# Performance work log

Hardware: AMD Instinct MI355X
Metric: run time of the kernel (lower is better)

Reference implementation:

```python
import jax, jax.numpy as jnp
import numpy as np


def setup_inputs() -> dict:
    key = jax.random.key(0)
    ks = jax.random.split(key, 10)
    B, T, F, C, D, O = 4, 1000, 257, 6, 2048, 2
    # target_doas in DEGREES (module multiplies by pi/180): azi in [0,360), zenith in [0,180)
    tdoa = jax.random.uniform(ks[2], (B, T, 2), dtype=jnp.float32) * jnp.array([360.0, 180.0], jnp.float32)
    # codebook dirs in RADIANS: azi in [0,2pi), zenith in [0,pi)
    dirs = jax.random.uniform(ks[3], (D, 2), dtype=jnp.float32) * jnp.array([2.0 * np.pi, np.pi], jnp.float32)
    return {
        "X_real": jax.random.normal(ks[0], (B, T, F, C), dtype=jnp.float32),
        "X_imag": jax.random.normal(ks[1], (B, T, F, C), dtype=jnp.float32),
        "target_doas": tdoa,
        "dirs": dirs,
        "w_conj_real": jax.random.normal(ks[4], (C, F, D), dtype=jnp.float32),
        "w_conj_imag": jax.random.normal(ks[5], (C, F, D), dtype=jnp.float32),
        "w_conj_ds_real": jax.random.normal(ks[6], (C, F, D), dtype=jnp.float32),
        "w_conj_ds_imag": jax.random.normal(ks[7], (C, F, D), dtype=jnp.float32),
        "w_binaural_real": jax.random.normal(ks[8], (O, F, D), dtype=jnp.float32),
        "w_binaural_imag": jax.random.normal(ks[9], (O, F, D), dtype=jnp.float32),
    }


def _as_ri(z):
    # complex -> stacked (real, imag) float array on last axis
    return jnp.stack([jnp.real(z), jnp.imag(z)], axis=-1)


def reference(X_real, X_imag, target_doas, dirs,
              w_conj_real, w_conj_imag,
              w_conj_ds_real, w_conj_ds_imag,
              w_binaural_real, w_binaural_imag):
    # --- angular (haversine) distance to direction codebook ---
    t = (jnp.pi / 180.0) * target_doas            # [B,T,2] radians
    azi_diff = t[..., 0][:, :, None] - dirs[:, 0][None, None, :]      # [B,T,D]
    zen_diff = t[..., 1][:, :, None] - dirs[:, 1][None, None, :]      # [B,T,D]
    a = jnp.sin(zen_diff / 2) ** 2 + \
        jnp.cos(t[..., 1])[:, :, None] * jnp.cos(dirs[:, 1])[None, None, :] * jnp.sin(azi_diff / 2) ** 2
    angle_diff = 2.0 * jnp.arcsin(jnp.sqrt(jnp.clip(a, 0.0, 1.0)))
    ind = jnp.argmin(angle_diff, axis=-1)          # [B,T] nearest-codebook index

    # --- gather complex beamformer weights by index: [C,F,D] -> [B,T,F,C] ---
    def gather(w):
        return jnp.transpose(w[:, :, ind], (2, 3, 1, 0))

    X = jax.lax.complex(X_real, X_imag)                                 # [B,T,F,C]
    w_conj = jax.lax.complex(gather(w_conj_real), gather(w_conj_imag))  # [B,T,F,C]
    w_ds = jax.lax.complex(gather(w_conj_ds_real), gather(w_conj_ds_imag))
    w_bin = jax.lax.complex(gather(w_binaural_real), gather(w_binaural_imag))  # [B,T,F,O]

    ds_multichannel_out = w_ds * X                 # [B,T,F,C]
    bf_out = jnp.sum(w_conj * X, axis=-1)          # [B,T,F]
    return (_as_ri(ds_multichannel_out), _as_ri(bf_out), _as_ri(w_bin))
```

## Files before the change

kernel.cpp:

```cpp
#include <hip/hip_runtime.h>
#include <math.h>

typedef float f4v __attribute__((ext_vector_type(4)));
typedef float f2v __attribute__((ext_vector_type(2)));

constexpr int Bn = 4, Tn = 1000, Fn = 257, Cn = 6, Dn = 2048, On = 2;
constexpr int BTn = Bn * Tn;
constexpr double DEG2RAD = 0.017453292519943295;

constexpr size_t OUT0_F = (size_t)BTn * Fn * Cn * 2;
constexpr size_t OUT1_F = (size_t)BTn * Fn * 2;

constexpr int DCH = 32;
constexpr int NCH = Dn / DCH;
constexpr int FCH = 8;
constexpr int RWS = FCH * Cn;
constexpr int FCB = 24;
constexpr int RWB = FCB * On;
constexpr int YCD = (Fn + FCH - 1) / FCH;
constexpr int YB  = (Fn + FCB - 1) / FCB;
constexpr int DPAD = 34;
constexpr int NT = 512;

constexpr size_t TAB_BYTES  = (size_t)4 * Dn * sizeof(double);
constexpr size_t BTT_PAD    = 131072;
constexpr size_t IND_BYTES  = 16384;
constexpr size_t BOFF_BYTES = 4096;
constexpr size_t BENT_BYTES = 16384;
constexpr size_t WS_NEEDED  = TAB_BYTES + BTT_PAD + IND_BYTES + BOFF_BYTES + BENT_BYTES;

__global__ __launch_bounds__(256) void build_tables(const float2* __restrict__ dirs,
                                                    const float* __restrict__ tdoa,
                                                    double* __restrict__ tab,
                                                    double* __restrict__ bttab) {
    int id = blockIdx.x * 256 + threadIdx.x;
    if (id < Dn) {
        float2 dr = dirs[id];
        double d0 = (double)dr.x, d1 = (double)dr.y;
        tab[0 * Dn + id] = cos(d0);
        tab[1 * Dn + id] = sin(d0);
        tab[2 * Dn + id] = cos(d1);
        tab[3 * Dn + id] = sin(d1);
    } else if (id < Dn + BTn) {
        int bt = id - Dn;
        double t0 = DEG2RAD * (double)tdoa[bt * 2 + 0];
        double t1 = DEG2RAD * (double)tdoa[bt * 2 + 1];
        bttab[bt * 4 + 0] = cos(t0);
        bttab[bt * 4 + 1] = sin(t0);
        bttab[bt * 4 + 2] = cos(t1);
        bttab[bt * 4 + 3] = sin(t1);
    }
}

__global__ __launch_bounds__(256) void argmin_lds(const double* __restrict__ bttab,
                                                  const double* __restrict__ tab,
                                                  int* __restrict__ ind) {
    __shared__ double s_cd0[Dn];
    __shared__ double s_sd0[Dn];
    __shared__ double s_cd1[Dn];
    __shared__ double s_sd1[Dn];
    const int t = threadIdx.x;
    #pragma unroll
    for (int k = 0; k < Dn / 256; ++k) {
        int d = t + 256 * k;
        s_cd0[d] = tab[0 * Dn + d];
        s_sd0[d] = tab[1 * Dn + d];
        s_cd1[d] = tab[2 * Dn + d];
        s_sd1[d] = tab[3 * Dn + d];
    }
    __syncthreads();
    const int w = t >> 6, lane = t & 63;
    #pragma unroll
    for (int s = 0; s < 4; ++s) {
        const int bt = blockIdx.x * 16 + w * 4 + s;
        double ct0 = bttab[bt * 4 + 0], st0 = bttab[bt * 4 + 1];
        double ct1 = bttab[bt * 4 + 2], st1 = bttab[bt * 4 + 3];
        double best = 1e300;
        int bidx = 0;
        for (int i = 0; i < Dn / 256; ++i) {
            const int d0 = lane + 256 * i;
            double a[4];
            #pragma unroll
            for (int k = 0; k < 4; ++k) {
                int d = d0 + 64 * k;
                double u  = ct1 * s_cd1[d];
                double m1 = 1.0 - (u + st1 * s_sd1[d]);
                double m0 = 1.0 - (ct0 * s_cd0[d] + st0 * s_sd0[d]);
                a[k] = m1 + u * m0;
            }
            #pragma unroll
            for (int k = 0; k < 4; ++k) {
                int d = d0 + 64 * k;
                if (a[k] < best) { best = a[k]; bidx = d; }
            }
        }
        #pragma unroll
        for (int off = 32; off > 0; off >>= 1) {
            double ov = __shfl_down(best, off);
            int oi = __shfl_down(bidx, off);
            if (ov < best || (ov == best && oi < bidx)) { best = ov; bidx = oi; }
        }
        if (lane == 0) ind[bt] = bidx;
    }
}

__global__ __launch_bounds__(256) void bucket_bts(const int* __restrict__ ind,
                                                  int* __restrict__ boff,
                                                  int* __restrict__ bent) {
    __shared__ int cnts[NCH];
    __shared__ int curs[NCH];
    const int t = threadIdx.x;
    if (t < NCH) cnts[t] = 0;
    __syncthreads();
    #pragma unroll
    for (int k = 0; k < (BTn + 255) / 256; ++k) {
        int bt = k * 256 + t;
        if (bt < BTn) atomicAdd(&cnts[ind[bt] >> 5], 1);
    }
    __syncthreads();
    if (t == 0) {
        int acc = 0;
        for (int i = 0; i < NCH; ++i) { curs[i] = acc; boff[i] = acc; acc += cnts[i]; }
        boff[NCH] = acc;
    }
    __syncthreads();
    #pragma unroll
    for (int k = 0; k < (BTn + 255) / 256; ++k) {
        int bt = k * 256 + t;
        if (bt < BTn) {
            int d = ind[bt];
            int p = atomicAdd(&curs[d >> 5], 1);
            bent[p] = (bt << 5) | (d & 31);
        }
    }
}

__global__ __launch_bounds__(NT) void fuse_all(
    const float* __restrict__ Xr, const float* __restrict__ Xi,
    const int* __restrict__ boff, const int* __restrict__ bent,
    const float* __restrict__ wcr, const float* __restrict__ wci,
    const float* __restrict__ wdr, const float* __restrict__ wdi,
    const float* __restrict__ wbr, const float* __restrict__ wbi,
    float* __restrict__ out0, float* __restrict__ out1, float* __restrict__ out2) {
    __shared__ __align__(16) char smem[2 * RWS * DPAD * sizeof(f2v)];
    const int bx = blockIdx.x;
    const int d0 = bx * DCH;
    const int t = threadIdx.x;
    const int off = boff[bx];
    const int cnt = boff[bx + 1] - off;

    if (blockIdx.y < YCD) {
        f2v (*tc)[DPAD] = (f2v(*)[DPAD])smem;
        f2v (*td)[DPAD] = (f2v(*)[DPAD])(smem + sizeof(f2v) * RWS * DPAD);
        const int f0 = blockIdx.y * FCH;
        const int items = cnt * FCH;

        bool vA = false; int btA = 0, fA = 0, dlA = 0, rbA = 0;
        f2v xrA0 = {0,0}, xrA1 = {0,0}, xrA2 = {0,0};
        f2v xiA0 = {0,0}, xiA1 = {0,0}, xiA2 = {0,0};
        if (t < items) {
            int e = bent[off + (t >> 3)];
            int fi = t & 7, f = f0 + fi;
            if (f < Fn) {
                vA = true; btA = e >> 5; fA = f; dlA = e & 31; rbA = fi * Cn;
                size_t xb = ((size_t)btA * Fn + f) * Cn;
                const f2v* xr2 = (const f2v*)(Xr + xb);
                const f2v* xi2 = (const f2v*)(Xi + xb);
                xrA0 = xr2[0]; xrA1 = xr2[1]; xrA2 = xr2[2];
                xiA0 = xi2[0]; xiA1 = xi2[1]; xiA2 = xi2[2];
            }
        }
        #pragma unroll
        for (int j = 0; j < 2; ++j) {
            int idx = j * NT + t;
            if (idx < 768) {
                const int pair = (idx >= 384) ? 1 : 0;
                int k = idx - pair * 384;
                int r = k >> 3, q4 = k & 7;
                int fi = r / Cn, c = r - fi * Cn;
                int f = f0 + fi;
                if (f < Fn) {
                    size_t s = (size_t)(c * Fn + f) * Dn + d0 + 4 * q4;
                    f4v vr = *(const f4v*)((pair ? wdr : wcr) + s);
                    f4v vi = *(const f4v*)((pair ? wdi : wci) + s);
                    f4v* trow = (f4v*)&(pair ? td : tc)[r][0];
                    f4v lo = {vr[0], vi[0], vr[1], vi[1]};
                    f4v hi = {vr[2], vi[2], vr[3], vi[3]};
                    trow[2 * q4]     = lo;
                    trow[2 * q4 + 1] = hi;
                }
            }
        }
        __syncthreads();

        for (int base = 0; base < items; base += NT) {
            bool vB = false; int btB = 0, fB = 0, dlB = 0, rbB = 0;
            f2v xrB0 = {0,0}, xrB1 = {0,0}, xrB2 = {0,0};
            f2v xiB0 = {0,0}, xiB1 = {0,0}, xiB2 = {0,0};
            int itn = base + NT + t;
            if (itn < items) {
                int e = bent[off + (itn >> 3)];
                int fi = itn & 7, f = f0 + fi;
                if (f < Fn) {
                    vB = true; btB = e >> 5; fB = f; dlB = e & 31; rbB = fi * Cn;
                    size_t xb = ((size_t)btB * Fn + f) * Cn;
                    const f2v* xr2 = (const f2v*)(Xr + xb);
                    const f2v* xi2 = (const f2v*)(Xi + xb);
                    xrB0 = xr2[0]; xrB1 = xr2[1]; xrB2 = xr2[2];
                    xiB0 = xi2[0]; xiB1 = xi2[1]; xiB2 = xi2[2];
                }
            }
            if (vA) {
                float xr[Cn] = {xrA0[0], xrA0[1], xrA1[0], xrA1[1], xrA2[0], xrA2[1]};
                float xi[Cn] = {xiA0[0], xiA0[1], xiA1[0], xiA1[1], xiA2[0], xiA2[1]};
                float o0[Cn * 2];
                float accr = 0.f, acci = 0.f;
                #pragma unroll
                for (int c = 0; c < Cn; ++c) {
                    f2v wcv = tc[rbA + c][dlA];
                    f2v wdv = td[rbA + c][dlA];
                    o0[2 * c]     = wdv[0] * xr[c] - wdv[1] * xi[c];
                    o0[2 * c + 1] = wdv[0] * xi[c] + wdv[1] * xr[c];
                    accr += wcv[0] * xr[c] - wcv[1] * xi[c];
                    acci += wcv[0] * xi[c] + wcv[1] * xr[c];
                }
                size_t xb = ((size_t)btA * Fn + fA) * Cn;
                f4v* ob = (f4v*)(out0 + xb * 2);
                f4v p0 = {o0[0], o0[1], o0[2], o0[3]};
                f4v p1 = {o0[4], o0[5], o0[6], o0[7]};
                f4v p2 = {o0[8], o0[9], o0[10], o0[11]};
                ob[0] = p0; ob[1] = p1; ob[2] = p2;
                f2v o1 = {accr, acci};
                ((f2v*)out1)[(size_t)btA * Fn + fA] = o1;
            }
            vA = vB; btA = btB; fA = fB; dlA = dlB; rbA = rbB;
            xrA0 = xrB0; xrA1 = xrB1; xrA2 = xrB2;
            xiA0 = xiB0; xiA1 = xiB1; xiA2 = xiB2;
        }
    } else {
        f2v (*tb)[DPAD] = (f2v(*)[DPAD])smem;
        const int f0 = (blockIdx.y - YCD) * FCB;
        {
            int idx = t;
            if (idx < RWB * 8) {
                int r = idx >> 3, q4 = idx & 7;
                int fi = r >> 1, o = r & 1;
                int f = f0 + fi;
                if (f < Fn) {
                    size_t s = (size_t)(o * Fn + f) * Dn + d0 + 4 * q4;
                    f4v vr = *(const f4v*)(wbr + s);
                    f4v vi = *(const f4v*)(wbi + s);
                    f4v* trow = (f4v*)&tb[r][0];
                    f4v lo = {vr[0], vi[0], vr[1], vi[1]};
                    f4v hi = {vr[2], vi[2], vr[3], vi[3]};
                    trow[2 * q4]     = lo;
                    trow[2 * q4 + 1] = hi;
                }
            }
        }
        __syncthreads();
        const int items = cnt * FCB;
        for (int base = 0; base < items; base += NT) {
            int it = base + t;
            if (it < items) {
                int m = it / FCB, fi = it - m * FCB;
                int e = bent[off + m];
                int bt = e >> 5, dl = e & 31;
                int f = f0 + fi;
                if (f < Fn) {
                    f2v a = tb[fi * 2][dl];
                    f2v b = tb[fi * 2 + 1][dl];
                    f4v o2 = {a[0], a[1], b[0], b[1]};
                    ((f4v*)out2)[(size_t)bt * Fn + f] = o2;
                }
            }
        }
    }
}

__global__ __launch_bounds__(256) void main_direct(
    const float* __restrict__ Xr, const float* __restrict__ Xi,
    const float* __restrict__ tdoa, const float2* __restrict__ dirs,
    const float* __restrict__ wcr, const float* __restrict__ wci,
    const float* __restrict__ wdr, const float* __restrict__ wdi,
    const float* __restrict__ wbr, const float* __restrict__ wbi,
    float2* __restrict__ out0, float2* __restrict__ out1, float2* __restrict__ out2) {
    const int bt = blockIdx.x;
    const int tid = threadIdx.x;
    __shared__ double sv[256];
    __shared__ int si[256];

    double t0 = DEG2RAD * (double)tdoa[bt * 2 + 0];
    double t1 = DEG2RAD * (double)tdoa[bt * 2 + 1];
    double ct1 = cos(t1);
    double best = 1e300;
    int bidx = 0;
    for (int d = tid; d < Dn; d += 256) {
        float2 dr = dirs[d];
        double s1 = sin(0.5 * (t1 - (double)dr.y));
        double s2 = sin(0.5 * (t0 - (double)dr.x));
        double a = s1 * s1 + ct1 * cos((double)dr.y) * (s2 * s2);
        if (a < best) { best = a; bidx = d; }
    }
    sv[tid] = best; si[tid] = bidx;
    __syncthreads();
    for (int s = 128; s > 0; s >>= 1) {
        if (tid < s) {
            double v = sv[tid + s]; int j = si[tid + s];
            if (v < sv[tid] || (v == sv[tid] && j < si[tid])) { sv[tid] = v; si[tid] = j; }
        }
        __syncthreads();
    }
    const int dsel = si[0];
    const size_t base = (size_t)bt * Fn * Cn;

    for (int f = tid; f < Fn; f += 256) {
        const int fc = f * Cn;
        float accr = 0.f, acci = 0.f;
        #pragma unroll
        for (int c = 0; c < Cn; ++c) {
            float xr = Xr[base + fc + c], xi = Xi[base + fc + c];
            size_t wo = (size_t)(c * Fn + f) * Dn + dsel;
            float a_ = wdr[wo], b_ = wdi[wo];
            out0[base + fc + c] = make_float2(a_ * xr - b_ * xi, a_ * xi + b_ * xr);
            float p = wcr[wo], q = wci[wo];
            accr += p * xr - q * xi;
            acci += p * xi + q * xr;
        }
        out1[(size_t)bt * Fn + f] = make_float2(accr, acci);
        #pragma unroll
        for (int o = 0; o < On; ++o) {
            size_t wo = (size_t)(o * Fn + f) * Dn + dsel;
            out2[((size_t)bt * Fn + f) * On + o] = make_float2(wbr[wo], wbi[wo]);
        }
    }
}

extern "C" void kernel_launch(void* const* d_in, const int* in_sizes, int n_in,
                              void* d_out, int out_size, void* d_ws, size_t ws_size,
                              hipStream_t stream) {
    const float* Xr   = (const float*)d_in[0];
    const float* Xi   = (const float*)d_in[1];
    const float* tdoa = (const float*)d_in[2];
    const float2* dirs = (const float2*)d_in[3];
    const float* wcr = (const float*)d_in[4];
    const float* wci = (const float*)d_in[5];
    const float* wdr = (const float*)d_in[6];
    const float* wdi = (const float*)d_in[7];
    const float* wbr = (const float*)d_in[8];
    const float* wbi = (const float*)d_in[9];

    float* out = (float*)d_out;

    if (ws_size >= WS_NEEDED) {
        char* ws = (char*)d_ws;
        double* tab   = (double*)ws;
        double* bttab = (double*)(ws + TAB_BYTES);
        int* ind  = (int*)(ws + TAB_BYTES + BTT_PAD);
        int* boff = (int*)(ws + TAB_BYTES + BTT_PAD + IND_BYTES);
        int* bent = (int*)(ws + TAB_BYTES + BTT_PAD + IND_BYTES + BOFF_BYTES);

        build_tables<<<(Dn + BTn + 255) / 256, 256, 0, stream>>>(dirs, tdoa, tab, bttab);
        argmin_lds<<<BTn / 16, 256, 0, stream>>>(bttab, tab, ind);
        bucket_bts<<<1, 256, 0, stream>>>(ind, boff, bent);
        dim3 g(NCH, YCD + YB);
        fuse_all<<<g, NT, 0, stream>>>(Xr, Xi, boff, bent,
                                       wcr, wci, wdr, wdi, wbr, wbi,
                                       out, out + OUT0_F, out + OUT0_F + OUT1_F);
    } else {
        main_direct<<<BTn, 256, 0, stream>>>(Xr, Xi, tdoa, dirs,
                                             wcr, wci, wdr, wdi, wbr, wbi,
                                             (float2*)out,
                                             (float2*)(out + OUT0_F),
                                             (float2*)(out + OUT0_F + OUT1_F));
    }
}
```

Before: 61.27 us.

## Process three frequency chunks per block with double-buffered weight tiles

Each fuse_all block for the ds/bf path now handles three consecutive 8-frequency chunks instead of one. It prefetches the next chunk's weights into registers while computing the current chunk, then writes them into an alternate LDS buffer. This cuts the block count in the y dimension by about three and hides weight-load latency behind compute. The cost is doubled LDS use per block (lower occupancy) and less grid parallelism, with extra syncs per step.

```diff
diff --git a/kernel.cpp b/kernel.cpp
--- a/kernel.cpp
+++ b/kernel.cpp
@@ -15,11 +15,14 @@
 constexpr int NCH = Dn / DCH;
 constexpr int FCH = 8;
 constexpr int RWS = FCH * Cn;
+constexpr int STEPS = 3;
+constexpr int FGRP = FCH * STEPS;
+constexpr int YCDP = (Fn + FGRP - 1) / FGRP;
 constexpr int FCB = 24;
 constexpr int RWB = FCB * On;
-constexpr int YCD = (Fn + FCH - 1) / FCH;
 constexpr int YB  = (Fn + FCB - 1) / FCB;
 constexpr int DPAD = 34;
+constexpr int TILE = RWS * DPAD;
 constexpr int NT = 512;
 
 constexpr size_t TAB_BYTES  = (size_t)4 * Dn * sizeof(double);
@@ -142,25 +145,49 @@
     const float* __restrict__ wdr, const float* __restrict__ wdi,
     const float* __restrict__ wbr, const float* __restrict__ wbi,
     float* __restrict__ out0, float* __restrict__ out1, float* __restrict__ out2) {
-    __shared__ __align__(16) char smem[2 * RWS * DPAD * sizeof(f2v)];
+    __shared__ __align__(16) f2v buf[2][2 * TILE];
     const int bx = blockIdx.x;
     const int d0 = bx * DCH;
     const int t = threadIdx.x;
     const int off = boff[bx];
     const int cnt = boff[bx + 1] - off;
 
-    if (blockIdx.y < YCD) {
-        f2v (*tc)[DPAD] = (f2v(*)[DPAD])smem;
-        f2v (*td)[DPAD] = (f2v(*)[DPAD])(smem + sizeof(f2v) * RWS * DPAD);
-        const int f0 = blockIdx.y * FCH;
+    if (blockIdx.y < YCDP) {
+        const int fbase = blockIdx.y * FGRP;
         const int items = cnt * FCH;
 
+        auto wsrc = [&](int pair, int re, int r, int q4, int f0) -> const f4v* {
+            int fi = r / Cn, c = r - fi * Cn;
+            int f = f0 + fi;
+            if (f >= Fn) return (const f4v*)nullptr;
+            const float* p = pair ? (re ? wdr : wdi) : (re ? wcr : wci);
+            return (const f4v*)(p + (size_t)(c * Fn + f) * Dn + d0 + 4 * q4);
+        };
+        const int i0 = t;
+        const int p0 = (i0 >= 384) ? 1 : 0;
+        const int k0 = i0 - p0 * 384, r0 = k0 >> 3, q0 = k0 & 7;
+        const int i1 = NT + t;
+        const bool h1 = (i1 < 768);
+        const int p1 = 1;
+        const int k1 = i1 - 384, r1 = k1 >> 3, q1 = k1 & 7;
+
+        f4v w0r = {0,0,0,0}, w0i = {0,0,0,0}, w1r = {0,0,0,0}, w1i = {0,0,0,0};
+        {
+            const f4v* a = wsrc(p0, 1, r0, q0, fbase);
+            const f4v* b = wsrc(p0, 0, r0, q0, fbase);
+            if (a) { w0r = *a; w0i = *b; }
+            if (h1) {
+                const f4v* c2 = wsrc(p1, 1, r1, q1, fbase);
+                const f4v* d2 = wsrc(p1, 0, r1, q1, fbase);
+                if (c2) { w1r = *c2; w1i = *d2; }
+            }
+        }
         bool vA = false; int btA = 0, fA = 0, dlA = 0, rbA = 0;
         f2v xrA0 = {0,0}, xrA1 = {0,0}, xrA2 = {0,0};
         f2v xiA0 = {0,0}, xiA1 = {0,0}, xiA2 = {0,0};
         if (t < items) {
             int e = bent[off + (t >> 3)];
-            int fi = t & 7, f = f0 + fi;
+            int fi = t & 7, f = fbase + fi;
             if (f < Fn) {
                 vA = true; btA = e >> 5; fA = f; dlA = e & 31; rbA = fi * Cn;
                 size_t xb = ((size_t)btA * Fn + f) * Cn;
@@ -170,76 +197,113 @@
                 xiA0 = xi2[0]; xiA1 = xi2[1]; xiA2 = xi2[2];
             }
         }
-        #pragma unroll
-        for (int j = 0; j < 2; ++j) {
-            int idx = j * NT + t;
-            if (idx < 768) {
-                const int pair = (idx >= 384) ? 1 : 0;
-                int k = idx - pair * 384;
-                int r = k >> 3, q4 = k & 7;
-                int fi = r / Cn, c = r - fi * Cn;
-                int f = f0 + fi;
-                if (f < Fn) {
-                    size_t s = (size_t)(c * Fn + f) * Dn + d0 + 4 * q4;
-                    f4v vr = *(const f4v*)((pair ? wdr : wcr) + s);
-                    f4v vi = *(const f4v*)((pair ? wdi : wci) + s);
-                    f4v* trow = (f4v*)&(pair ? td : tc)[r][0];
-                    f4v lo = {vr[0], vi[0], vr[1], vi[1]};
-                    f4v hi = {vr[2], vi[2], vr[3], vi[3]};
-                    trow[2 * q4]     = lo;
-                    trow[2 * q4 + 1] = hi;
-                }
+        {
+            f4v* row0 = (f4v*)&buf[0][p0 * TILE + r0 * DPAD];
+            f4v lo0 = {w0r[0], w0i[0], w0r[1], w0i[1]};
+            f4v hi0 = {w0r[2], w0i[2], w0r[3], w0i[3]};
+            row0[2 * q0] = lo0; row0[2 * q0 + 1] = hi0;
+            if (h1) {
+                f4v* row1 = (f4v*)&buf[0][p1 * TILE + r1 * DPAD];
+                f4v lo1 = {w1r[0], w1i[0], w1r[1], w1i[1]};
+                f4v hi1 = {w1r[2], w1i[2], w1r[3], w1i[3]};
+                row1[2 * q1] = lo1; row1[2 * q1 + 1] = hi1;
             }
         }
         __syncthreads();
 
-        for (int base = 0; base < items; base += NT) {
-            bool vB = false; int btB = 0, fB = 0, dlB = 0, rbB = 0;
-            f2v xrB0 = {0,0}, xrB1 = {0,0}, xrB2 = {0,0};
-            f2v xiB0 = {0,0}, xiB1 = {0,0}, xiB2 = {0,0};
-            int itn = base + NT + t;
-            if (itn < items) {
-                int e = bent[off + (itn >> 3)];
-                int fi = itn & 7, f = f0 + fi;
-                if (f < Fn) {
-                    vB = true; btB = e >> 5; fB = f; dlB = e & 31; rbB = fi * Cn;
-                    size_t xb = ((size_t)btB * Fn + f) * Cn;
-                    const f2v* xr2 = (const f2v*)(Xr + xb);
-                    const f2v* xi2 = (const f2v*)(Xi + xb);
-                    xrB0 = xr2[0]; xrB1 = xr2[1]; xrB2 = xr2[2];
-                    xiB0 = xi2[0]; xiB1 = xi2[1]; xiB2 = xi2[2];
-                }
-            }
-            if (vA) {
-                float xr[Cn] = {xrA0[0], xrA0[1], xrA1[0], xrA1[1], xrA2[0], xrA2[1]};
-                float xi[Cn] = {xiA0[0], xiA0[1], xiA1[0], xiA1[1], xiA2[0], xiA2[1]};
-                float o0[Cn * 2];
-                float accr = 0.f, acci = 0.f;
-                #pragma unroll
-                for (int c = 0; c < Cn; ++c) {
-                    f2v wcv = tc[rbA + c][dlA];
-                    f2v wdv = td[rbA + c][dlA];
-                    o0[2 * c]     = wdv[0] * xr[c] - wdv[1] * xi[c];
-                    o0[2 * c + 1] = wdv[0] * xi[c] + wdv[1] * xr[c];
-                    accr += wcv[0] * xr[c] - wcv[1] * xi[c];
-                    acci += wcv[0] * xi[c] + wcv[1] * xr[c];
-                }
-                size_t xb = ((size_t)btA * Fn + fA) * Cn;
-                f4v* ob = (f4v*)(out0 + xb * 2);
-                f4v p0 = {o0[0], o0[1], o0[2], o0[3]};
-                f4v p1 = {o0[4], o0[5], o0[6], o0[7]};
-                f4v p2 = {o0[8], o0[9], o0[10], o0[11]};
-                ob[0] = p0; ob[1] = p1; ob[2] = p2;
-                f2v o1 = {accr, acci};
-                ((f2v*)out1)[(size_t)btA * Fn + fA] = o1;
-            }
-            vA = vB; btA = btB; fA = fB; dlA = dlB; rbA = rbB;
-            xrA0 = xrB0; xrA1 = xrB1; xrA2 = xrB2;
-            xiA0 = xiB0; xiA1 = xiB1; xiA2 = xiB2;
+        for (int s = 0; s < STEPS; ++s) {
+            const int f0 = fbase + s * FCH;
+            const f2v* tc = &buf[s & 1][0];
+            const f2v* td = &buf[s & 1][TILE];
+            const bool more = (s + 1 < STEPS);
+
+            f4v nw0r = {0,0,0,0}, nw0i = {0,0,0,0}, nw1r = {0,0,0,0}, nw1i = {0,0,0,0};
+            if (more) {
+                const f4v* a = wsrc(p0, 1, r0, q0, f0 + FCH);
+                const f4v* b = wsrc(p0, 0, r0, q0, f0 + FCH);
+                if (a) { nw0r = *a; nw0i = *b; }
+                if (h1) {
+                    const f4v* c2 = wsrc(p1, 1, r1, q1, f0 + FCH);
+                    const f4v* d2 = wsrc(p1, 0, r1, q1, f0 + FCH);
+                    if (c2) { nw1r = *c2; nw1i = *d2; }
+                }
+            }
+
+            for (int base = 0; base < items; base += NT) {
+                bool vB = false; int btB = 0, fB = 0, dlB = 0, rbB = 0;
+                f2v xrB0 = {0,0}, xrB1 = {0,0}, xrB2 = {0,0};
+                f2v xiB0 = {0,0}, xiB1 = {0,0}, xiB2 = {0,0};
+                int itn = base + NT + t;
+                if (itn < items) {
+                    int e = bent[off + (itn >> 3)];
+                    int fi = itn & 7, f = f0 + fi;
+                    if (f < Fn) {
+                        vB = true; btB = e >> 5; fB = f; dlB = e & 31; rbB = fi * Cn;
+                        size_t xb = ((size_t)btB * Fn + f) * Cn;
+                        const f2v* xr2 = (const f2v*)(Xr + xb);
+                        const f2v* xi2 = (const f2v*)(Xi + xb);
+                        xrB0 = xr2[0]; xrB1 = xr2[1]; xrB2 = xr2[2];
+                        xiB0 = xi2[0]; xiB1 = xi2[1]; xiB2 = xi2[2];
+                    }
+                }
+                if (vA) {
+                    float xr[Cn] = {xrA0[0], xrA0[1], xrA1[0], xrA1[1], xrA2[0], xrA2[1]};
+                    float xi[Cn] = {xiA0[0], xiA0[1], xiA1[0], xiA1[1], xiA2[0], xiA2[1]};
+                    float o0[Cn * 2];
+                    float accr = 0.f, acci = 0.f;
+                    #pragma unroll
+                    for (int c = 0; c < Cn; ++c) {
+                        f2v wcv = tc[(rbA + c) * DPAD + dlA];
+                        f2v wdv = td[(rbA + c) * DPAD + dlA];
+                        o0[2 * c]     = wdv[0] * xr[c] - wdv[1] * xi[c];
+                        o0[2 * c + 1] = wdv[0] * xi[c] + wdv[1] * xr[c];
+                        accr += wcv[0] * xr[c] - wcv[1] * xi[c];
+                        acci += wcv[0] * xi[c] + wcv[1] * xr[c];
+                    }
+                    size_t xb = ((size_t)btA * Fn + fA) * Cn;
+                    f4v* ob = (f4v*)(out0 + xb * 2);
+                    f4v pp0 = {o0[0], o0[1], o0[2], o0[3]};
+                    f4v pp1 = {o0[4], o0[5], o0[6], o0[7]};
+                    f4v pp2 = {o0[8], o0[9], o0[10], o0[11]};
+                    ob[0] = pp0; ob[1] = pp1; ob[2] = pp2;
+                    f2v o1 = {accr, acci};
+                    ((f2v*)out1)[(size_t)btA * Fn + fA] = o1;
+                }
+                vA = vB; btA = btB; fA = fB; dlA = dlB; rbA = rbB;
+                xrA0 = xrB0; xrA1 = xrB1; xrA2 = xrB2;
+                xiA0 = xiB0; xiA1 = xiB1; xiA2 = xiB2;
+            }
+
+            if (more) {
+                vA = false;
+                if (t < items) {
+                    int e = bent[off + (t >> 3)];
+                    int fi = t & 7, f = f0 + FCH + fi;
+                    if (f < Fn) {
+                        vA = true; btA = e >> 5; fA = f; dlA = e & 31; rbA = fi * Cn;
+                        size_t xb = ((size_t)btA * Fn + f) * Cn;
+                        const f2v* xr2 = (const f2v*)(Xr + xb);
+                        const f2v* xi2 = (const f2v*)(Xi + xb);
+                        xrA0 = xr2[0]; xrA1 = xr2[1]; xrA2 = xr2[2];
+                        xiA0 = xi2[0]; xiA1 = xi2[1]; xiA2 = xi2[2];
+                    }
+                }
+                f4v* row0 = (f4v*)&buf[(s + 1) & 1][p0 * TILE + r0 * DPAD];
+                f4v lo0 = {nw0r[0], nw0i[0], nw0r[1], nw0i[1]};
+                f4v hi0 = {nw0r[2], nw0i[2], nw0r[3], nw0i[3]};
+                row0[2 * q0] = lo0; row0[2 * q0 + 1] = hi0;
+                if (h1) {
+                    f4v* row1 = (f4v*)&buf[(s + 1) & 1][p1 * TILE + r1 * DPAD];
+                    f4v lo1 = {nw1r[0], nw1i[0], nw1r[1], nw1i[1]};
+                    f4v hi1 = {nw1r[2], nw1i[2], nw1r[3], nw1i[3]};
+                    row1[2 * q1] = lo1; row1[2 * q1 + 1] = hi1;
+                }
+                __syncthreads();
+            }
         }
     } else {
-        f2v (*tb)[DPAD] = (f2v(*)[DPAD])smem;
-        const int f0 = (blockIdx.y - YCD) * FCB;
+        f2v* tb = &buf[0][0];
+        const int f0 = (blockIdx.y - YCDP) * FCB;
         {
             int idx = t;
             if (idx < RWB * 8) {
@@ -250,7 +314,7 @@
                     size_t s = (size_t)(o * Fn + f) * Dn + d0 + 4 * q4;
                     f4v vr = *(const f4v*)(wbr + s);
                     f4v vi = *(const f4v*)(wbi + s);
-                    f4v* trow = (f4v*)&tb[r][0];
+                    f4v* trow = (f4v*)&tb[r * DPAD];
                     f4v lo = {vr[0], vi[0], vr[1], vi[1]};
                     f4v hi = {vr[2], vi[2], vr[3], vi[3]};
                     trow[2 * q4]     = lo;
@@ -268,8 +332,8 @@
                 int bt = e >> 5, dl = e & 31;
                 int f = f0 + fi;
                 if (f < Fn) {
-                    f2v a = tb[fi * 2][dl];
-                    f2v b = tb[fi * 2 + 1][dl];
+                    f2v a = tb[(fi * 2) * DPAD + dl];
+                    f2v b = tb[(fi * 2 + 1) * DPAD + dl];
                     f4v o2 = {a[0], a[1], b[0], b[1]};
                     ((f4v*)out2)[(size_t)bt * Fn + f] = o2;
                 }
@@ -363,7 +427,7 @@
         build_tables<<<(Dn + BTn + 255) / 256, 256, 0, stream>>>(dirs, tdoa, tab, bttab);
         argmin_lds<<<BTn / 16, 256, 0, stream>>>(bttab, tab, ind);
         bucket_bts<<<1, 256, 0, stream>>>(ind, boff, bent);
-        dim3 g(NCH, YCD + YB);
+        dim3 g(NCH, YCDP + YB);
         fuse_all<<<g, NT, 0, stream>>>(Xr, Xi, boff, bent,
                                        wcr, wci, wdr, wdi, wbr, wbi,
                                        out, out + OUT0_F, out + OUT0_F + OUT1_F);
```

New measurement: 68.23 us. 11.4% more time.
